# Performance work log

Hardware: AMD Instinct MI355X
Metric: run time of the kernel (lower is better)

Reference implementation:

```python
import jax, jax.numpy as jnp
import numpy as np

DIM = 2048
NUM_HEADS = 16
HEAD_DIM = 128
MAX_SEQ_LEN = 2048
ATTN_SCALE = 0.12
EPS = 1e-6


def _rms_norm(x):
    # RMSNorm without learned weight, over last dim
    return x * jax.lax.rsqrt(jnp.mean(jnp.square(x), axis=-1, keepdims=True) + EPS)


def _rope_tables(T):
    # half of the head dim rotates, half is identity (zero frequency)
    quarter = HEAD_DIM // 4
    angular_freq = (1.0 / 1024.0) ** jnp.linspace(0.0, 1.0, quarter, dtype=jnp.float32)
    angular_freq = jnp.concatenate([angular_freq, jnp.zeros(quarter, dtype=jnp.float32)])  # [D/2]
    t = jnp.arange(T, dtype=jnp.float32)
    theta = t[:, None] * angular_freq[None, :]  # [T, D/2]
    return jnp.cos(theta), jnp.sin(theta)


def _apply_rope(x, cos, sin):
    # x: [B, T, H, D]; cos/sin: [T, D/2] -> broadcast [1, T, 1, D/2]
    x1, x2 = jnp.split(x, 2, axis=-1)
    c = cos[None, :, None, :]
    s = sin[None, :, None, :]
    y1 = x1 * c + x2 * s
    y2 = -x1 * s + x2 * c
    return jnp.concatenate([y1, y2], axis=-1)


def setup_inputs() -> dict:
    key = jax.random.key(0)
    k1, k2, k3, k4 = jax.random.split(key, 4)
    hdim = NUM_HEADS * HEAD_DIM
    x = jax.random.normal(k1, (1, MAX_SEQ_LEN, DIM), dtype=jnp.float32)
    qkvo_w = jax.random.normal(k2, (4, hdim, DIM), dtype=jnp.float32) * (DIM ** -0.5)
    ve = jax.random.normal(k3, (1, MAX_SEQ_LEN, hdim), dtype=jnp.float32)
    lambdas = jax.random.uniform(k4, (2,), dtype=jnp.float32)
    return {"x": x, "qkvo_w": qkvo_w, "ve": ve, "lambdas": lambdas}


def reference(x, qkvo_w, ve, lambdas):
    B, T, _ = x.shape
    H, D = NUM_HEADS, HEAD_DIM
    # fused qkv projection: [B, T, 3*H*D]
    qkv = jnp.einsum('btc,ehc->bteh', x, qkvo_w[:3]).reshape(B, T, 3, H, D)
    q, k, v = qkv[:, :, 0], qkv[:, :, 1], qkv[:, :, 2]  # each [B, T, H, D]
    q, k, v = _rms_norm(q), _rms_norm(k), _rms_norm(v)
    cos, sin = _rope_tables(T)
    q = _apply_rope(q, cos, sin)
    k = _apply_rope(k, cos, sin)
    v = lambdas[0] * v + lambdas[1] * ve.reshape(B, T, H, D)
    # causal attention with fixed scale
    scores = jnp.einsum('bthd,bshd->bhts', q, k) * ATTN_SCALE  # [B, H, T, T]
    causal = jnp.tril(jnp.ones((T, T), dtype=bool))
    scores = jnp.where(causal[None, None], scores, -jnp.inf)
    p = jax.nn.softmax(scores, axis=-1)
    y = jnp.einsum('bhts,bshd->bthd', p, v).reshape(B, T, H * D)
    return jnp.einsum('bth,ch->btc', y, qkvo_w[3])
```

## Files before the change

kernel.cpp:

```cpp
#include <hip/hip_runtime.h>
#include <math.h>

#define SEQ  2048
#define CDIM 2048
#define NH   16
#define DH   128
#define HDIM 2048

typedef __attribute__((ext_vector_type(8))) short  bf16x8;
typedef __attribute__((ext_vector_type(4))) float  f32x4;
typedef unsigned short ushort_t;

__device__ __forceinline__ unsigned short f2bf(float f) {
  unsigned u = __float_as_uint(f);
  u = (u + 0x7fffu + ((u >> 16) & 1u)) >> 16;
  return (unsigned short)u;
}
__device__ __forceinline__ float b2f(unsigned short s) {
  return __uint_as_float((unsigned)s << 16);
}

__device__ __forceinline__ void async_ld16(const ushort_t* g, ushort_t* l) {
  __builtin_amdgcn_global_load_lds((const __attribute__((address_space(1))) unsigned int*)g,
                                   (__attribute__((address_space(3))) unsigned int*)l,
                                   16, 0, 0);
}

__device__ __forceinline__ f32x4 mfma16(bf16x8 a, bf16x8 b, f32x4 c) {
  return __builtin_amdgcn_mfma_f32_16x16x32_bf16(a, b, c, 0, 0, 0);
}

__global__ __launch_bounds__(256) void to_bf16(const float* __restrict__ src,
                                               ushort_t* __restrict__ dst, int n8) {
  int i = blockIdx.x * 256 + threadIdx.x;
  if (i >= n8) return;
  const float4* s = (const float4*)src;
  float4 f0 = s[i * 2], f1 = s[i * 2 + 1];
  bf16x8 o;
  o[0] = (short)f2bf(f0.x); o[1] = (short)f2bf(f0.y);
  o[2] = (short)f2bf(f0.z); o[3] = (short)f2bf(f0.w);
  o[4] = (short)f2bf(f1.x); o[5] = (short)f2bf(f1.y);
  o[6] = (short)f2bf(f1.z); o[7] = (short)f2bf(f1.w);
  *(bf16x8*)&dst[i * 8] = o;
}

template <int OUT_BF16>
__global__ __launch_bounds__(256) void gemm_bf16(const ushort_t* __restrict__ A,
                                                 const ushort_t* __restrict__ B,
                                                 void* __restrict__ Cv,
                                                 long bStride, long cStride) {
  constexpr int K = CDIM, N = HDIM;
  __shared__ __align__(16) ushort_t As[2][128 * 32];
  __shared__ __align__(16) ushort_t Bs[2][128 * 32];
  const ushort_t* Bp = B + (long)blockIdx.z * bStride;
  const int m0 = blockIdx.y * 128, n0 = blockIdx.x * 128;
  const int tid = threadIdx.x, lane = tid & 63, wave = tid >> 6;
  const int wm = wave >> 1, wn = wave & 1;
  const int g = lane >> 4, l15 = lane & 15;
  const int srow = tid >> 2, scc = tid & 3;

  f32x4 acc[4][4];
#pragma unroll
  for (int i = 0; i < 4; ++i)
#pragma unroll
    for (int j = 0; j < 4; ++j) acc[i][j] = (f32x4)0.0f;

  auto stage = [&](int buf, int k0) {
    int r0 = srow, r1 = srow + 64;
    int c0 = scc ^ ((r0 >> 1) & 3), c1 = scc ^ ((r1 >> 1) & 3);
    async_ld16(&A [(long)(m0 + r0) * K + k0 + c0 * 8], &As[buf][wave * 512]);
    async_ld16(&A [(long)(m0 + r1) * K + k0 + c1 * 8], &As[buf][2048 + wave * 512]);
    async_ld16(&Bp[(long)(n0 + r0) * K + k0 + c0 * 8], &Bs[buf][wave * 512]);
    async_ld16(&Bp[(long)(n0 + r1) * K + k0 + c1 * 8], &Bs[buf][2048 + wave * 512]);
  };

  stage(0, 0);
  int cur = 0;
  for (int k0 = 0; k0 < K; k0 += 32) {
    __syncthreads();
    if (k0 + 32 < K) stage(cur ^ 1, k0 + 32);

    bf16x8 af[4], bfr[4];
#pragma unroll
    for (int mi = 0; mi < 4; ++mi) {
      int row = wm * 64 + mi * 16 + l15;
      int cc = g ^ ((row >> 1) & 3);
      af[mi] = *(const bf16x8*)&As[cur][row * 32 + cc * 8];
    }
#pragma unroll
    for (int ni = 0; ni < 4; ++ni) {
      int row = wn * 64 + ni * 16 + l15;
      int cc = g ^ ((row >> 1) & 3);
      bfr[ni] = *(const bf16x8*)&Bs[cur][row * 32 + cc * 8];
    }
#pragma unroll
    for (int mi = 0; mi < 4; ++mi)
#pragma unroll
      for (int ni = 0; ni < 4; ++ni)
        acc[mi][ni] = mfma16(af[mi], bfr[ni], acc[mi][ni]);
    cur ^= 1;
  }

#pragma unroll
  for (int mi = 0; mi < 4; ++mi)
#pragma unroll
    for (int ni = 0; ni < 4; ++ni) {
      int row = m0 + wm * 64 + mi * 16 + g * 4;
      int col = n0 + wn * 64 + ni * 16 + l15;
#pragma unroll
      for (int r = 0; r < 4; ++r) {
        if (OUT_BF16)
          ((ushort_t*)Cv)[cStride * blockIdx.z + (long)(row + r) * N + col] = f2bf(acc[mi][ni][r]);
        else
          ((float*)Cv)[(long)(row + r) * N + col] = acc[mi][ni][r];
      }
    }
}

__global__ __launch_bounds__(256) void gemm_out64(const ushort_t* __restrict__ A,
                                                  const ushort_t* __restrict__ B,
                                                  float* __restrict__ C) {
  constexpr int K = CDIM, N = HDIM;
  __shared__ __align__(16) ushort_t As[2][64 * 32];
  __shared__ __align__(16) ushort_t Bs[2][128 * 32];
  const int m0 = blockIdx.y * 64, n0 = blockIdx.x * 128;
  const int tid = threadIdx.x, lane = tid & 63, wave = tid >> 6;
  const int wm = wave >> 1, wn = wave & 1;
  const int g = lane >> 4, l15 = lane & 15;
  const int srow = tid >> 2, scc = tid & 3;

  f32x4 acc[2][4];
#pragma unroll
  for (int i = 0; i < 2; ++i)
#pragma unroll
    for (int j = 0; j < 4; ++j) acc[i][j] = (f32x4)0.0f;

  auto stage = [&](int buf, int k0) {
    int ca = scc ^ ((srow >> 1) & 3);
    async_ld16(&A[(long)(m0 + srow) * K + k0 + ca * 8], &As[buf][wave * 512]);
    int r1 = srow + 64;
    int c0 = scc ^ ((srow >> 1) & 3), c1 = scc ^ ((r1 >> 1) & 3);
    async_ld16(&B[(long)(n0 + srow) * K + k0 + c0 * 8], &Bs[buf][wave * 512]);
    async_ld16(&B[(long)(n0 + r1) * K + k0 + c1 * 8], &Bs[buf][2048 + wave * 512]);
  };

  stage(0, 0);
  int cur = 0;
  for (int k0 = 0; k0 < K; k0 += 32) {
    __syncthreads();
    if (k0 + 32 < K) stage(cur ^ 1, k0 + 32);

    bf16x8 af[2], bfr[4];
#pragma unroll
    for (int mi = 0; mi < 2; ++mi) {
      int row = wm * 32 + mi * 16 + l15;
      int cc = g ^ ((row >> 1) & 3);
      af[mi] = *(const bf16x8*)&As[cur][row * 32 + cc * 8];
    }
#pragma unroll
    for (int ni = 0; ni < 4; ++ni) {
      int row = wn * 64 + ni * 16 + l15;
      int cc = g ^ ((row >> 1) & 3);
      bfr[ni] = *(const bf16x8*)&Bs[cur][row * 32 + cc * 8];
    }
#pragma unroll
    for (int mi = 0; mi < 2; ++mi)
#pragma unroll
      for (int ni = 0; ni < 4; ++ni)
        acc[mi][ni] = mfma16(af[mi], bfr[ni], acc[mi][ni]);
    cur ^= 1;
  }

#pragma unroll
  for (int mi = 0; mi < 2; ++mi)
#pragma unroll
    for (int ni = 0; ni < 4; ++ni) {
      int row = m0 + wm * 32 + mi * 16 + g * 4;
      int col = n0 + wn * 64 + ni * 16 + l15;
#pragma unroll
      for (int r = 0; r < 4; ++r)
        C[(long)(row + r) * N + col] = acc[mi][ni][r];
    }
}

__device__ __forceinline__ float wave_sum64(float x) {
#pragma unroll
  for (int m = 32; m >= 1; m >>= 1) x += __shfl_xor(x, m, 64);
  return x;
}

__global__ __launch_bounds__(256) void norm_rope(ushort_t* __restrict__ qkvb,
                                                 const float* __restrict__ ve,
                                                 const float* __restrict__ lambdas) {
  const int gid = blockIdx.x * 4 + (threadIdx.x >> 6);
  const int t = gid >> 4, h = gid & 15;
  const int d = threadIdx.x & 63;
  const long base = (long)t * HDIM + h * DH;
  ushort_t* q = qkvb + base;
  ushort_t* k = qkvb + (long)SEQ * HDIM + base;
  ushort_t* v = qkvb + 2L * SEQ * HDIM + base;

  float q1 = b2f(q[d]), q2 = b2f(q[d + 64]);
  float k1 = b2f(k[d]), k2 = b2f(k[d + 64]);
  float v1 = b2f(v[d]), v2 = b2f(v[d + 64]);

  float qsc = rsqrtf(wave_sum64(q1 * q1 + q2 * q2) * (1.0f / 128.0f) + 1e-6f);
  float ksc = rsqrtf(wave_sum64(k1 * k1 + k2 * k2) * (1.0f / 128.0f) + 1e-6f);
  float vsc = rsqrtf(wave_sum64(v1 * v1 + v2 * v2) * (1.0f / 128.0f) + 1e-6f);
  q1 *= qsc; q2 *= qsc;
  k1 *= ksc; k2 *= ksc;
  v1 *= vsc; v2 *= vsc;

  float freq = (d < 32) ? powf(1.0f / 1024.0f, (float)d * (1.0f / 31.0f)) : 0.0f;
  float th = (float)t * freq;
  float c = cosf(th), s = sinf(th);

  float qo1 = q1 * c + q2 * s, qo2 = -q1 * s + q2 * c;
  float ko1 = k1 * c + k2 * s, ko2 = -k1 * s + k2 * c;

  float l0 = lambdas[0], l1 = lambdas[1];
  const float* vep = ve + base;
  float vo1 = l0 * v1 + l1 * vep[d];
  float vo2 = l0 * v2 + l1 * vep[d + 64];

  q[d] = f2bf(qo1); q[d + 64] = f2bf(qo2);
  k[d] = f2bf(ko1); k[d + 64] = f2bf(ko2);
  v[d] = f2bf(vo1); v[d + 64] = f2bf(vo2);
}

__global__ __launch_bounds__(256) void transpose_v(const ushort_t* __restrict__ vb,
                                                   ushort_t* __restrict__ vbT) {
  __shared__ __align__(16) ushort_t L[64 * 136];
  const int t0 = blockIdx.x * 64, h = blockIdx.y;
  const int tid = threadIdx.x;
#pragma unroll
  for (int p = 0; p < 4; ++p) {
    int idx = p * 256 + tid;
    int row = idx >> 4, cc = idx & 15;
    *(bf16x8*)&L[row * 136 + cc * 8] =
        *(const bf16x8*)&vb[(long)(t0 + row) * HDIM + h * DH + cc * 8];
  }
  __syncthreads();
#pragma unroll
  for (int p = 0; p < 4; ++p) {
    int idx = p * 256 + tid;
    int d = idx >> 3, tc = (idx & 7) * 8;
    bf16x8 o;
#pragma unroll
    for (int j = 0; j < 8; ++j) o[j] = (short)L[(tc + j) * 136 + d];
    *(bf16x8*)&vbT[((long)h * DH + d) * SEQ + t0 + tc] = o;
  }
}

__global__ __launch_bounds__(256) void flash_mfma(const ushort_t* __restrict__ qkvb,
                                                  const ushort_t* __restrict__ vbT,
                                                  ushort_t* __restrict__ yb) {
  __shared__ __align__(16) ushort_t Ks[2][64 * 128];
  __shared__ __align__(16) ushort_t Vt[2][128 * 64];
  __shared__ __align__(16) ushort_t Ps[64 * 72];
  const int h = blockIdx.y;
  const int qi = (h < 8) ? blockIdx.x : (31 - blockIdx.x);
  const int q0 = qi * 64;
  const int tid = threadIdx.x, lane = tid & 63, wave = tid >> 6;
  const int g = lane >> 4, l15 = lane & 15;
  const ushort_t* Kg = qkvb + (long)SEQ * HDIM;
  const ushort_t* Vg = vbT + (long)h * DH * SEQ;

  bf16x8 qf[4];
#pragma unroll
  for (int ks = 0; ks < 4; ++ks)
    qf[ks] = *(const bf16x8*)
        &qkvb[(long)(q0 + wave * 16 + l15) * HDIM + h * DH + ks * 32 + g * 8];

  f32x4 oacc[8];
#pragma unroll
  for (int dt = 0; dt < 8; ++dt) oacc[dt] = (f32x4)0.0f;
  float mrow = -1e30f, lrow = 0.0f;

  auto stage = [&](int buf, int s0) {
#pragma unroll
    for (int i = 0; i < 4; ++i) {
      int idx = i * 256 + tid;
      { int row = idx >> 4, cc = idx & 15, cg = cc ^ (row & 7);
        async_ld16(&Kg[(long)(s0 + row) * HDIM + h * DH + cg * 8],
                   &Ks[buf][i * 2048 + wave * 512]); }
      { int row = idx >> 3, cc = idx & 7,  cg = cc ^ (row & 7);
        async_ld16(&Vg[(long)row * SEQ + s0 + cg * 8],
                   &Vt[buf][i * 2048 + wave * 512]); }
    }
  };

  stage(0, 0);
  int cur = 0;
  for (int s0 = 0; s0 <= q0; s0 += 64) {
    __syncthreads();
    if (s0 + 64 <= q0) stage(cur ^ 1, s0 + 64);

    f32x4 st[4];
#pragma unroll
    for (int mt = 0; mt < 4; ++mt) st[mt] = (f32x4)0.0f;
    __builtin_amdgcn_s_setprio(1);
#pragma unroll
    for (int ks = 0; ks < 4; ++ks)
#pragma unroll
      for (int mt = 0; mt < 4; ++mt) {
        int row = mt * 16 + l15;
        int cc = (ks * 4 + g) ^ (row & 7);
        bf16x8 a = *(const bf16x8*)&Ks[cur][row * 128 + cc * 8];
        st[mt] = mfma16(a, qf[ks], st[mt]);
      }
    __builtin_amdgcn_s_setprio(0);

    const int qg = q0 + wave * 16 + l15;
    float p[4][4];
#pragma unroll
    for (int mt = 0; mt < 4; ++mt)
#pragma unroll
      for (int r = 0; r < 4; ++r) p[mt][r] = st[mt][r] * 0.12f;
    if (s0 == q0) {
#pragma unroll
      for (int mt = 0; mt < 4; ++mt)
#pragma unroll
        for (int r = 0; r < 4; ++r)
          if (s0 + mt * 16 + g * 4 + r > qg) p[mt][r] = -1e30f;
    }
    float tmax = -1e30f;
#pragma unroll
    for (int mt = 0; mt < 4; ++mt)
#pragma unroll
      for (int r = 0; r < 4; ++r) tmax = fmaxf(tmax, p[mt][r]);
    tmax = fmaxf(tmax, __shfl_xor(tmax, 16, 64));
    tmax = fmaxf(tmax, __shfl_xor(tmax, 32, 64));
    float nm = fmaxf(mrow, tmax);
    float alpha = __expf(mrow - nm);
    float psum = 0.0f;
#pragma unroll
    for (int mt = 0; mt < 4; ++mt) {
      float e0 = __expf(p[mt][0] - nm), e1 = __expf(p[mt][1] - nm);
      float e2 = __expf(p[mt][2] - nm), e3 = __expf(p[mt][3] - nm);
      unsigned short b0 = f2bf(e0), b1 = f2bf(e1), b2 = f2bf(e2), b3 = f2bf(e3);
      psum += b2f(b0) + b2f(b1) + b2f(b2) + b2f(b3);
      unsigned lo = (unsigned)b0 | ((unsigned)b1 << 16);
      unsigned hi = (unsigned)b2 | ((unsigned)b3 << 16);
      *(uint2*)&Ps[(wave * 16 + l15) * 72 + mt * 16 + g * 4] = make_uint2(lo, hi);
    }
    psum += __shfl_xor(psum, 16, 64);
    psum += __shfl_xor(psum, 32, 64);
    mrow = nm;
    lrow = lrow * alpha + psum;

    float aO[4];
#pragma unroll
    for (int r = 0; r < 4; ++r) aO[r] = __shfl(alpha, g * 4 + r, 64);
#pragma unroll
    for (int dt = 0; dt < 8; ++dt)
#pragma unroll
      for (int r = 0; r < 4; ++r) oacc[dt][r] *= aO[r];

    __builtin_amdgcn_s_setprio(1);
#pragma unroll
    for (int ks = 0; ks < 2; ++ks) {
      bf16x8 ap = *(const bf16x8*)&Ps[(wave * 16 + l15) * 72 + ks * 32 + g * 8];
#pragma unroll
      for (int dt = 0; dt < 8; ++dt) {
        int row = dt * 16 + l15;
        int cc = (ks * 4 + g) ^ (row & 7);
        bf16x8 bv = *(const bf16x8*)&Vt[cur][row * 64 + cc * 8];
        oacc[dt] = mfma16(ap, bv, oacc[dt]);
      }
    }
    __builtin_amdgcn_s_setprio(0);
    cur ^= 1;
  }

  float linv[4];
#pragma unroll
  for (int r = 0; r < 4; ++r) linv[r] = 1.0f / __shfl(lrow, g * 4 + r, 64);
#pragma unroll
  for (int dt = 0; dt < 8; ++dt) {
    int row = q0 + wave * 16 + g * 4;
    int col = h * DH + dt * 16 + l15;
#pragma unroll
    for (int r = 0; r < 4; ++r)
      yb[(long)(row + r) * HDIM + col] = f2bf(oacc[dt][r] * linv[r]);
  }
}

extern "C" void kernel_launch(void* const* d_in, const int* in_sizes, int n_in,
                              void* d_out, int out_size, void* d_ws, size_t ws_size,
                              hipStream_t stream) {
  const float* x       = (const float*)d_in[0];
  const float* w       = (const float*)d_in[1];
  const float* ve      = (const float*)d_in[2];
  const float* lambdas = (const float*)d_in[3];
  float* out = (float*)d_out;

  char* ws = (char*)d_ws;
  ushort_t* qkvb = (ushort_t*)ws;
  ushort_t* xb   = (ushort_t*)(ws + 25165824);
  ushort_t* wb   = (ushort_t*)(ws + 33554432);
  ushort_t* vbT  = (ushort_t*)(ws + 67108864);
  ushort_t* yb   = xb;

  to_bf16<<<2048, 256, 0, stream>>>(x, xb, (SEQ * CDIM) / 8);
  to_bf16<<<8192, 256, 0, stream>>>(w, wb, (4 * HDIM * CDIM) / 8);
  gemm_bf16<1><<<dim3(16, 16, 3), 256, 0, stream>>>(xb, wb, qkvb,
                                                    (long)HDIM * CDIM, (long)SEQ * HDIM);
  norm_rope<<<(SEQ * NH) / 4, 256, 0, stream>>>(qkvb, ve, lambdas);
  transpose_v<<<dim3(SEQ / 64, NH), 256, 0, stream>>>(qkvb + 2L * SEQ * HDIM, vbT);
  flash_mfma<<<dim3(SEQ / 64, NH), 256, 0, stream>>>(qkvb, vbT, yb);
  gemm_out64<<<dim3(16, 32), 256, 0, stream>>>(yb, wb + 3L * HDIM * CDIM, out);
}
```

Measured before the change: 319.9 us.

## Fuse RMSNorm/RoPE/value-mix into QKV GEMM epilogue; split-K the output projection

The QKV GEMM now gives each block one full head (128 columns) and remaps the B fragments so each lane holds both rotary halves. RMSNorm, RoPE and the value-embedding mix are then applied in the epilogue, which drops the separate norm_rope kernel and its bf16 read-modify-write of q/k/v. The output projection changes from 64-row tiles to 128-row tiles with split-K over two halves. The second partial is written to workspace and added by a new addf4 kernel, which costs an extra fp32 write and read of the output.

```diff
diff --git a/kernel.cpp b/kernel.cpp
--- a/kernel.cpp
+++ b/kernel.cpp
@@ -44,16 +44,17 @@
   *(bf16x8*)&dst[i * 8] = o;
 }
 
-template <int OUT_BF16>
-__global__ __launch_bounds__(256) void gemm_bf16(const ushort_t* __restrict__ A,
-                                                 const ushort_t* __restrict__ B,
-                                                 void* __restrict__ Cv,
-                                                 long bStride, long cStride) {
-  constexpr int K = CDIM, N = HDIM;
+__global__ __launch_bounds__(256) void gemm_qkv_fused(const ushort_t* __restrict__ A,
+                                                      const ushort_t* __restrict__ W,
+                                                      ushort_t* __restrict__ qkvb,
+                                                      const float* __restrict__ ve,
+                                                      const float* __restrict__ lambdas) {
+  constexpr int K = CDIM;
   __shared__ __align__(16) ushort_t As[2][128 * 32];
   __shared__ __align__(16) ushort_t Bs[2][128 * 32];
-  const ushort_t* Bp = B + (long)blockIdx.z * bStride;
-  const int m0 = blockIdx.y * 128, n0 = blockIdx.x * 128;
+  const int z = blockIdx.z, h = blockIdx.x;
+  const ushort_t* Bp = W + (long)z * HDIM * CDIM;
+  const int m0 = blockIdx.y * 128, n0 = h * DH;
   const int tid = threadIdx.x, lane = tid & 63, wave = tid >> 6;
   const int wm = wave >> 1, wn = wave & 1;
   const int g = lane >> 4, l15 = lane & 15;
@@ -89,7 +90,7 @@
     }
 #pragma unroll
     for (int ni = 0; ni < 4; ++ni) {
-      int row = wn * 64 + ni * 16 + l15;
+      int row = wn * 32 + (ni & 1) * 16 + (ni >> 1) * 64 + l15;
       int cc = g ^ ((row >> 1) & 3);
       bfr[ni] = *(const bf16x8*)&Bs[cur][row * 32 + cc * 8];
     }
@@ -101,59 +102,114 @@
     cur ^= 1;
   }
 
+  __syncthreads();
+  float* SS = (float*)As;
+
+  float sc[4][4];
 #pragma unroll
   for (int mi = 0; mi < 4; ++mi)
 #pragma unroll
-    for (int ni = 0; ni < 4; ++ni) {
-      int row = m0 + wm * 64 + mi * 16 + g * 4;
-      int col = n0 + wn * 64 + ni * 16 + l15;
+    for (int r = 0; r < 4; ++r) {
+      float s = 0.0f;
+#pragma unroll
+      for (int ni = 0; ni < 4; ++ni) s += acc[mi][ni][r] * acc[mi][ni][r];
+      s += __shfl_xor(s, 1, 64); s += __shfl_xor(s, 2, 64);
+      s += __shfl_xor(s, 4, 64); s += __shfl_xor(s, 8, 64);
+      if (l15 == 0) SS[wn * 128 + wm * 64 + mi * 16 + g * 4 + r] = s;
+    }
+  __syncthreads();
+#pragma unroll
+  for (int mi = 0; mi < 4; ++mi)
+#pragma unroll
+    for (int r = 0; r < 4; ++r) {
+      int row = wm * 64 + mi * 16 + g * 4 + r;
+      float tot = SS[row] + SS[128 + row];
+      sc[mi][r] = rsqrtf(tot * (1.0f / 128.0f) + 1e-6f);
+    }
+
+  if (z < 2) {
+    const int d0 = wn * 32 + l15;
+    float freq0 = (d0 < 32) ? powf(1.0f / 1024.0f, (float)d0 * (1.0f / 31.0f)) : 0.0f;
+    float freq1 = (d0 + 16 < 32) ? powf(1.0f / 1024.0f, (float)(d0 + 16) * (1.0f / 31.0f)) : 0.0f;
+#pragma unroll
+    for (int mi = 0; mi < 4; ++mi)
 #pragma unroll
       for (int r = 0; r < 4; ++r) {
-        if (OUT_BF16)
-          ((ushort_t*)Cv)[cStride * blockIdx.z + (long)(row + r) * N + col] = f2bf(acc[mi][ni][r]);
-        else
-          ((float*)Cv)[(long)(row + r) * N + col] = acc[mi][ni][r];
+        int t = m0 + wm * 64 + mi * 16 + g * 4 + r;
+        float scv = sc[mi][r];
+        long base = ((long)z * SEQ + t) * HDIM + n0;
+#pragma unroll
+        for (int ni = 0; ni < 2; ++ni) {
+          float fr = ni ? freq1 : freq0;
+          float th = (float)t * fr;
+          float c = cosf(th), s = sinf(th);
+          float x1 = acc[mi][ni][r] * scv;
+          float x2 = acc[mi][ni + 2][r] * scv;
+          int col = wn * 32 + ni * 16 + l15;
+          qkvb[base + col]      = f2bf(x1 * c + x2 * s);
+          qkvb[base + col + 64] = f2bf(x2 * c - x1 * s);
+        }
       }
-    }
-}
-
-__global__ __launch_bounds__(256) void gemm_out64(const ushort_t* __restrict__ A,
-                                                  const ushort_t* __restrict__ B,
-                                                  float* __restrict__ C) {
-  constexpr int K = CDIM, N = HDIM;
-  __shared__ __align__(16) ushort_t As[2][64 * 32];
+  } else {
+    float l0 = lambdas[0], l1 = lambdas[1];
+#pragma unroll
+    for (int mi = 0; mi < 4; ++mi)
+#pragma unroll
+      for (int r = 0; r < 4; ++r) {
+        int t = m0 + wm * 64 + mi * 16 + g * 4 + r;
+        float scv = sc[mi][r];
+        const float* vep = ve + (long)t * HDIM + n0;
+        long base = (2L * SEQ + t) * HDIM + n0;
+#pragma unroll
+        for (int ni = 0; ni < 4; ++ni) {
+          int col = wn * 32 + (ni & 1) * 16 + (ni >> 1) * 64 + l15;
+          float vo = l0 * (acc[mi][ni][r] * scv) + l1 * vep[col];
+          qkvb[base + col] = f2bf(vo);
+        }
+      }
+  }
+}
+
+__global__ __launch_bounds__(256) void gemm_out_ks(const ushort_t* __restrict__ A,
+                                                   const ushort_t* __restrict__ B,
+                                                   float* __restrict__ C0,
+                                                   float* __restrict__ C1) {
+  constexpr int K = CDIM, N = HDIM, KH = CDIM / 2;
+  __shared__ __align__(16) ushort_t As[2][128 * 32];
   __shared__ __align__(16) ushort_t Bs[2][128 * 32];
-  const int m0 = blockIdx.y * 64, n0 = blockIdx.x * 128;
+  const int kb = blockIdx.z * KH;
+  float* C = blockIdx.z ? C1 : C0;
+  const int m0 = blockIdx.y * 128, n0 = blockIdx.x * 128;
   const int tid = threadIdx.x, lane = tid & 63, wave = tid >> 6;
   const int wm = wave >> 1, wn = wave & 1;
   const int g = lane >> 4, l15 = lane & 15;
   const int srow = tid >> 2, scc = tid & 3;
 
-  f32x4 acc[2][4];
-#pragma unroll
-  for (int i = 0; i < 2; ++i)
+  f32x4 acc[4][4];
+#pragma unroll
+  for (int i = 0; i < 4; ++i)
 #pragma unroll
     for (int j = 0; j < 4; ++j) acc[i][j] = (f32x4)0.0f;
 
   auto stage = [&](int buf, int k0) {
-    int ca = scc ^ ((srow >> 1) & 3);
-    async_ld16(&A[(long)(m0 + srow) * K + k0 + ca * 8], &As[buf][wave * 512]);
-    int r1 = srow + 64;
-    int c0 = scc ^ ((srow >> 1) & 3), c1 = scc ^ ((r1 >> 1) & 3);
-    async_ld16(&B[(long)(n0 + srow) * K + k0 + c0 * 8], &Bs[buf][wave * 512]);
-    async_ld16(&B[(long)(n0 + r1) * K + k0 + c1 * 8], &Bs[buf][2048 + wave * 512]);
+    int r0 = srow, r1 = srow + 64;
+    int c0 = scc ^ ((r0 >> 1) & 3), c1 = scc ^ ((r1 >> 1) & 3);
+    async_ld16(&A[(long)(m0 + r0) * K + kb + k0 + c0 * 8], &As[buf][wave * 512]);
+    async_ld16(&A[(long)(m0 + r1) * K + kb + k0 + c1 * 8], &As[buf][2048 + wave * 512]);
+    async_ld16(&B[(long)(n0 + r0) * K + kb + k0 + c0 * 8], &Bs[buf][wave * 512]);
+    async_ld16(&B[(long)(n0 + r1) * K + kb + k0 + c1 * 8], &Bs[buf][2048 + wave * 512]);
   };
 
   stage(0, 0);
   int cur = 0;
-  for (int k0 = 0; k0 < K; k0 += 32) {
+  for (int k0 = 0; k0 < KH; k0 += 32) {
     __syncthreads();
-    if (k0 + 32 < K) stage(cur ^ 1, k0 + 32);
-
-    bf16x8 af[2], bfr[4];
-#pragma unroll
-    for (int mi = 0; mi < 2; ++mi) {
-      int row = wm * 32 + mi * 16 + l15;
+    if (k0 + 32 < KH) stage(cur ^ 1, k0 + 32);
+
+    bf16x8 af[4], bfr[4];
+#pragma unroll
+    for (int mi = 0; mi < 4; ++mi) {
+      int row = wm * 64 + mi * 16 + l15;
       int cc = g ^ ((row >> 1) & 3);
       af[mi] = *(const bf16x8*)&As[cur][row * 32 + cc * 8];
     }
@@ -164,7 +220,7 @@
       bfr[ni] = *(const bf16x8*)&Bs[cur][row * 32 + cc * 8];
     }
 #pragma unroll
-    for (int mi = 0; mi < 2; ++mi)
+    for (int mi = 0; mi < 4; ++mi)
 #pragma unroll
       for (int ni = 0; ni < 4; ++ni)
         acc[mi][ni] = mfma16(af[mi], bfr[ni], acc[mi][ni]);
@@ -172,10 +228,10 @@
   }
 
 #pragma unroll
-  for (int mi = 0; mi < 2; ++mi)
+  for (int mi = 0; mi < 4; ++mi)
 #pragma unroll
     for (int ni = 0; ni < 4; ++ni) {
-      int row = m0 + wm * 32 + mi * 16 + g * 4;
+      int row = m0 + wm * 64 + mi * 16 + g * 4;
       int col = n0 + wn * 64 + ni * 16 + l15;
 #pragma unroll
       for (int r = 0; r < 4; ++r)
@@ -183,49 +239,13 @@
     }
 }
 
-__device__ __forceinline__ float wave_sum64(float x) {
-#pragma unroll
-  for (int m = 32; m >= 1; m >>= 1) x += __shfl_xor(x, m, 64);
-  return x;
-}
-
-__global__ __launch_bounds__(256) void norm_rope(ushort_t* __restrict__ qkvb,
-                                                 const float* __restrict__ ve,
-                                                 const float* __restrict__ lambdas) {
-  const int gid = blockIdx.x * 4 + (threadIdx.x >> 6);
-  const int t = gid >> 4, h = gid & 15;
-  const int d = threadIdx.x & 63;
-  const long base = (long)t * HDIM + h * DH;
-  ushort_t* q = qkvb + base;
-  ushort_t* k = qkvb + (long)SEQ * HDIM + base;
-  ushort_t* v = qkvb + 2L * SEQ * HDIM + base;
-
-  float q1 = b2f(q[d]), q2 = b2f(q[d + 64]);
-  float k1 = b2f(k[d]), k2 = b2f(k[d + 64]);
-  float v1 = b2f(v[d]), v2 = b2f(v[d + 64]);
-
-  float qsc = rsqrtf(wave_sum64(q1 * q1 + q2 * q2) * (1.0f / 128.0f) + 1e-6f);
-  float ksc = rsqrtf(wave_sum64(k1 * k1 + k2 * k2) * (1.0f / 128.0f) + 1e-6f);
-  float vsc = rsqrtf(wave_sum64(v1 * v1 + v2 * v2) * (1.0f / 128.0f) + 1e-6f);
-  q1 *= qsc; q2 *= qsc;
-  k1 *= ksc; k2 *= ksc;
-  v1 *= vsc; v2 *= vsc;
-
-  float freq = (d < 32) ? powf(1.0f / 1024.0f, (float)d * (1.0f / 31.0f)) : 0.0f;
-  float th = (float)t * freq;
-  float c = cosf(th), s = sinf(th);
-
-  float qo1 = q1 * c + q2 * s, qo2 = -q1 * s + q2 * c;
-  float ko1 = k1 * c + k2 * s, ko2 = -k1 * s + k2 * c;
-
-  float l0 = lambdas[0], l1 = lambdas[1];
-  const float* vep = ve + base;
-  float vo1 = l0 * v1 + l1 * vep[d];
-  float vo2 = l0 * v2 + l1 * vep[d + 64];
-
-  q[d] = f2bf(qo1); q[d + 64] = f2bf(qo2);
-  k[d] = f2bf(ko1); k[d + 64] = f2bf(ko2);
-  v[d] = f2bf(vo1); v[d + 64] = f2bf(vo2);
+__global__ __launch_bounds__(256) void addf4(float* __restrict__ out,
+                                             const float* __restrict__ part, int n4) {
+  int i = blockIdx.x * 256 + threadIdx.x;
+  if (i >= n4) return;
+  float4 a = ((const float4*)out)[i], b = ((const float4*)part)[i];
+  a.x += b.x; a.y += b.y; a.z += b.z; a.w += b.w;
+  ((float4*)out)[i] = a;
 }
 
 __global__ __launch_bounds__(256) void transpose_v(const ushort_t* __restrict__ vb,
@@ -401,13 +421,13 @@
   ushort_t* wb   = (ushort_t*)(ws + 33554432);
   ushort_t* vbT  = (ushort_t*)(ws + 67108864);
   ushort_t* yb   = xb;
+  float* part1   = (float*)ws;
 
   to_bf16<<<2048, 256, 0, stream>>>(x, xb, (SEQ * CDIM) / 8);
   to_bf16<<<8192, 256, 0, stream>>>(w, wb, (4 * HDIM * CDIM) / 8);
-  gemm_bf16<1><<<dim3(16, 16, 3), 256, 0, stream>>>(xb, wb, qkvb,
-                                                    (long)HDIM * CDIM, (long)SEQ * HDIM);
-  norm_rope<<<(SEQ * NH) / 4, 256, 0, stream>>>(qkvb, ve, lambdas);
+  gemm_qkv_fused<<<dim3(16, 16, 3), 256, 0, stream>>>(xb, wb, qkvb, ve, lambdas);
   transpose_v<<<dim3(SEQ / 64, NH), 256, 0, stream>>>(qkvb + 2L * SEQ * HDIM, vbT);
   flash_mfma<<<dim3(SEQ / 64, NH), 256, 0, stream>>>(qkvb, vbT, yb);
-  gemm_out64<<<dim3(16, 32), 256, 0, stream>>>(yb, wb + 3L * HDIM * CDIM, out);
-}
+  gemm_out_ks<<<dim3(16, 16, 2), 256, 0, stream>>>(yb, wb + 3L * HDIM * CDIM, out, part1);
+  addf4<<<4096, 256, 0, stream>>>(out, part1, (SEQ * CDIM) / 4);
+}
```

Result: slower. 694.9 us (+117.2%).
